# Kernel tuning notes

Measured on AMD Instinct MI355X. Metric: run time of the kernel, lower is better.

Reference implementation:

```python
import jax, jax.numpy as jnp
import numpy as np

T, B, E, H, DFF, K = 1024, 4, 512, 8, 2048, 31
D = E // H  # head_dim


def double_swish(x):
    # DoubleSwish: x * sigmoid(x - 1)
    return x * jax.nn.sigmoid(x - 1.0)


def ffn(x, w1, b1, w2, b2):
    # ScaledLinear -> ActivationBalancer(identity in eval) -> DoubleSwish -> ScaledLinear
    return double_swish(x @ w1.T + b1) @ w2.T + b2


def rel_shift(x):
    # x: (B, H, T, 2T-1) -> (B, H, T, T); out[b,h,i,j] = x[b,h,i, (T-1) - i + j]
    t = x.shape[2]
    idx = (t - 1) - jnp.arange(t)[:, None] + jnp.arange(t)[None, :]  # (T, T)
    return jnp.take_along_axis(x, idx[None, None], axis=-1)


def self_attn(x, pos_emb, wqkv, bqkv, wo, bo, wpos, u, v):
    # x: (T, B, E); Transformer-XL style rel-pos multi-head attention
    t, b, e = x.shape
    qkv = x @ wqkv.T + bqkv                       # (T, B, 3E)
    q, k, val = jnp.split(qkv, 3, axis=-1)
    q = q * (D ** -0.5)
    to_heads = lambda z: z.reshape(t, b, H, D).transpose(1, 2, 0, 3)  # (B,H,T,D)
    q, k, val = to_heads(q), to_heads(k), to_heads(val)
    # positional projection: (1, 2T-1, E) -> (1, H, D, 2T-1)
    p = (pos_emb @ wpos.T).reshape(1, 2 * t - 1, H, D).transpose(0, 2, 3, 1)
    ac = jnp.einsum('bhld,bhsd->bhls', q + u[None, :, None, :], k)
    bd = jnp.einsum('bhld,bhdm->bhlm', q + v[None, :, None, :], p)
    scores = ac + rel_shift(bd)                   # (B, H, T, T)
    attn = jax.nn.softmax(scores, axis=-1)
    out = jnp.einsum('bhls,bhsd->bhld', attn, val)
    out = out.transpose(2, 0, 1, 3).reshape(t, b, e)  # (T, B, E)
    return out @ wo.T + bo


def conv_module(x, pw1_w, pw1_b, dw_w, dw_b, pw2_w, pw2_b):
    # x: (T, B, C) -> (B, C, T)
    x = x.transpose(1, 2, 0)
    x = jnp.einsum('oc,bct->bot', pw1_w, x) + pw1_b[None, :, None]  # (B, 2C, T)
    a, g = jnp.split(x, 2, axis=1)
    x = a * jax.nn.sigmoid(g)                     # GLU over channel dim
    pad = (K - 1) // 2
    x = jax.lax.conv_general_dilated(
        x, dw_w, window_strides=(1,), padding=[(pad, pad)],
        dimension_numbers=('NCH', 'OIH', 'NCH'), feature_group_count=E)
    x = double_swish(x + dw_b[None, :, None])
    x = jnp.einsum('oc,bct->bot', pw2_w, x) + pw2_b[None, :, None]
    return x.transpose(2, 0, 1)                   # (T, B, C)


def basic_norm(x, log_eps):
    # BasicNorm: x * (mean(x^2, -1) + exp(eps))^{-0.5}
    return x * jax.lax.rsqrt(jnp.mean(x * x, axis=-1, keepdims=True) + jnp.exp(log_eps))


def setup_inputs() -> dict:
    key = jax.random.key(0)
    ks = jax.random.split(key, 24)
    std = jnp.float32(0.02)
    f = lambda k, s: jax.random.normal(k, s, jnp.float32)
    return dict(
        src=f(ks[0], (T, B, E)),
        pos_emb=f(ks[1], (1, 2 * T - 1, E)),
        in_proj_w=f(ks[2], (3 * E, E)) * std,
        in_proj_b=f(ks[3], (3 * E,)) * std,
        out_proj_w=f(ks[4], (E, E)) * std,
        out_proj_b=f(ks[5], (E,)) * std,
        linear_pos_w=f(ks[6], (E, E)) * std,
        pos_bias_u=f(ks[7], (H, D)) * jnp.float32(0.01),
        pos_bias_v=f(ks[8], (H, D)) * jnp.float32(0.01),
        ffm_w1=f(ks[9], (DFF, E)) * std, ffm_b1=f(ks[10], (DFF,)) * std,
        ffm_w2=f(ks[11], (E, DFF)) * std, ffm_b2=f(ks[12], (E,)) * std,
        ff_w1=f(ks[13], (DFF, E)) * std, ff_b1=f(ks[14], (DFF,)) * std,
        ff_w2=f(ks[15], (E, DFF)) * std, ff_b2=f(ks[16], (E,)) * std,
        conv_pw1_w=f(ks[17], (2 * E, E)) * std, conv_pw1_b=f(ks[18], (2 * E,)) * std,
        conv_dw_w=f(ks[19], (E, 1, K)) * std, conv_dw_b=f(ks[20], (E,)) * std,
        conv_pw2_w=f(ks[21], (E, E)) * std, conv_pw2_b=f(ks[22], (E,)) * std,
        norm_eps=jnp.array(np.log(0.25), jnp.float32),
    )


def reference(src, pos_emb, in_proj_w, in_proj_b, out_proj_w, out_proj_b,
              linear_pos_w, pos_bias_u, pos_bias_v,
              ffm_w1, ffm_b1, ffm_w2, ffm_b2,
              ff_w1, ff_b1, ff_w2, ff_b2,
              conv_pw1_w, conv_pw1_b, conv_dw_w, conv_dw_b, conv_pw2_w, conv_pw2_b,
              norm_eps):
    # macaron FFN
    x = src + ffn(src, ffm_w1, ffm_b1, ffm_w2, ffm_b2)
    # rel-pos self-attention
    x = x + self_attn(x, pos_emb, in_proj_w, in_proj_b, out_proj_w, out_proj_b,
                      linear_pos_w, pos_bias_u, pos_bias_v)
    # convolution module
    x = x + conv_module(x, conv_pw1_w, conv_pw1_b, conv_dw_w, conv_dw_b, conv_pw2_w, conv_pw2_b)
    # second FFN
    x = x + ffn(x, ff_w1, ff_b1, ff_w2, ff_b2)
    # balancer is identity in eval; final BasicNorm
    return basic_norm(x, norm_eps)
```

## Files before the change

kernel.cpp:

```cpp
#include <hip/hip_runtime.h>
#include <string.h>


#define T_ 1024
#define B_ 4
#define E_ 512
#define H_ 8
#define DFF_ 2048
#define KW_ 31

typedef unsigned short u16;
typedef unsigned int u32;
typedef __bf16 bf16x8 __attribute__((ext_vector_type(8)));
typedef float floatx4 __attribute__((ext_vector_type(4)));

__device__ __forceinline__ float b2f(u16 u) {
    return __uint_as_float(((u32)u) << 16);
}
__device__ __forceinline__ u16 f2b(float f) {
    u32 i = __float_as_uint(f);
    u32 r = (i + 0x7fffu + ((i >> 16) & 1u)) >> 16;
    return (u16)r;
}

__device__ __forceinline__ void glds16(const u16 *g, u16 *l) {
    __builtin_amdgcn_global_load_lds((const __attribute__((address_space(1))) void *)g,
                                     (__attribute__((address_space(3))) void *)l, 16, 0, 0);
}

__global__ __launch_bounds__(256) void fill_k(float *out, long long n, float val) {
    long long g = (long long)blockIdx.x * 256 + threadIdx.x;
    if (g < n) out[g] = val;
}

__global__ __launch_bounds__(256) void detect_k(const u16 *src16, int *flag) {
    __shared__ int sh[256];
    int tid = threadIdx.x;
    int cnt = 0;
    for (int i = tid; i < 4096; i += 256) {
        u16 x = src16[2 * i];
        int e = (x >> 7) & 0xFF;
        cnt += (e == 0 || (e >= 0x70 && e <= 0x8F)) ? 1 : 0;
    }
    sh[tid] = cnt;
    __syncthreads();
    for (int s = 128; s; s >>= 1) {
        if (tid < s) sh[tid] += sh[tid + s];
        __syncthreads();
    }
    if (tid == 0) *flag = (sh[0] < 2048) ? 1 : 0;
}

struct CVT {
    const void *in[24];
    long long pre[25];
};

__global__ __launch_bounds__(256) void convert_k(CVT c, u16 *dst, const int *flag,
                                                 long long total) {
    long long g8 = ((long long)blockIdx.x * 256 + threadIdx.x) * 8;
    if (g8 >= total) return;
    int s = 0;
#pragma unroll
    for (int i = 1; i < 25; i++) s += (g8 >= c.pre[i]) ? 1 : 0;
    long long l = g8 - c.pre[s];
    int f = *flag;
    if (g8 + 8 <= c.pre[s + 1]) {
        if (f) {
            const float *sp = (const float *)c.in[s] + l;
            float4 v0 = *(const float4 *)sp;
            float4 v1 = *(const float4 *)(sp + 4);
            uint4 o;
            o.x = (u32)f2b(v0.x) | ((u32)f2b(v0.y) << 16);
            o.y = (u32)f2b(v0.z) | ((u32)f2b(v0.w) << 16);
            o.z = (u32)f2b(v1.x) | ((u32)f2b(v1.y) << 16);
            o.w = (u32)f2b(v1.z) | ((u32)f2b(v1.w) << 16);
            *(uint4 *)(dst + g8) = o;
        } else {
            *(uint4 *)(dst + g8) = *(const uint4 *)((const u16 *)c.in[s] + l);
        }
    } else {
        for (int j = 0; j < 8; j++) {
            long long ge = g8 + j;
            if (ge >= total) break;
            int se = 0;
#pragma unroll
            for (int i = 1; i < 25; i++) se += (ge >= c.pre[i]) ? 1 : 0;
            long long le = ge - c.pre[se];
            dst[ge] = f ? f2b(((const float *)c.in[se])[le]) : ((const u16 *)c.in[se])[le];
        }
    }
}

struct GP {
    const u16 *A, *B;
    u16 *C;
    const u16 *bias;
    const void *resin;
    float *xr;
    u16 *xb;
    const u16 *ub, *vb;
    u16 *qu, *qv, *kh, *vt;
    int M, N, K, lda, ldb, ldc, mode, qcols, resin_f32;
    float qscale;
};

__device__ __forceinline__ void nt64_body(const GP &p, u16 *As, u16 *Bs,
                                          int bx, int by, int gx, int nb) {
    const int tid = threadIdx.x;
    const int wv = tid >> 6, ln = tid & 63;
    const int l16 = ln & 15, quad = ln >> 4;
    const int wm = (wv >> 2) << 5;
    const int wn = (wv & 3) << 4;
    const int lid = by * gx + bx;
    const int nid = (lid & 7) * (nb >> 3) + (lid >> 3);
    const int m0 = (nid / gx) << 6, n0 = (nid % gx) << 6;
    floatx4 zero = {0.f, 0.f, 0.f, 0.f};
    floatx4 acc[2];
    acc[0] = zero;
    acc[1] = zero;

    const int NT = p.K >> 6;

    const int srow = tid >> 3;
    const int sg = ((tid & 7) ^ (srow & 7)) << 3;
    int ra = m0 + srow;
    if (ra > p.M - 1) ra = p.M - 1;
    const u16 *Agp = p.A + (long long)ra * p.lda + sg;
    const u16 *Bgp = p.B + (long long)(n0 + srow) * p.ldb + sg;

    auto stage = [&](int bidx, int t) {
        const int k0 = t << 6;
        const int o = bidx << 12;
        glds16(Agp + k0, As + o + tid * 8);
        glds16(Bgp + k0, Bs + o + tid * 8);
    };
    auto ldregs = [&](int bidx, bf16x8 *af, bf16x8 *bv) {
        const int o = bidx << 12;
#pragma unroll
        for (int kk = 0; kk < 2; kk++) {
            const int swz = ((((kk << 2) | quad) ^ (l16 & 7)) << 3);
            bv[kk] = __builtin_bit_cast(bf16x8,
                *(const uint4 *)&Bs[o + ((wn + l16) << 6) + swz]);
#pragma unroll
            for (int mt = 0; mt < 2; mt++)
                af[kk * 2 + mt] = __builtin_bit_cast(bf16x8,
                    *(const uint4 *)&As[o + ((wm + (mt << 4) + l16) << 6) + swz]);
        }
    };
    auto mma = [&](const bf16x8 *af, const bf16x8 *bv) {
#pragma unroll
        for (int kk = 0; kk < 2; kk++)
#pragma unroll
            for (int mt = 0; mt < 2; mt++)
                acc[mt] = __builtin_amdgcn_mfma_f32_16x16x32_bf16(af[kk * 2 + mt], bv[kk],
                                                                  acc[mt], 0, 0, 0);
    };

    stage(0, 0);
    stage(1, 1);
    stage(2, 2);
    stage(3, 3);
    asm volatile("s_waitcnt vmcnt(4)" ::: "memory");
    __builtin_amdgcn_s_barrier();

    const int NP = NT >> 1;
    for (int ph = 0; ph < NP; ph++) {
        const int b0 = (ph << 1) & 3;
        bf16x8 af0[4], bv0[2], af1[4], bv1[2];
        ldregs(b0, af0, bv0);
        ldregs(b0 | 1, af1, bv1);
        __builtin_amdgcn_sched_barrier(0);
        asm volatile("s_waitcnt lgkmcnt(0)" ::: "memory");
        __builtin_amdgcn_s_barrier();
        __builtin_amdgcn_sched_barrier(0);
        const bool do_stage = (ph + 2 < NP);
        if (do_stage) {
            stage(b0, (ph << 1) + 4);
            stage(b0 | 1, (ph << 1) + 5);
        }
        mma(af0, bv0);
        mma(af1, bv1);
        if (ph + 1 < NP) {
            __builtin_amdgcn_sched_barrier(0);
            if (do_stage) {
                asm volatile("s_waitcnt vmcnt(4)" ::: "memory");
            } else {
                asm volatile("s_waitcnt vmcnt(0)" ::: "memory");
            }
            __builtin_amdgcn_s_barrier();
            __builtin_amdgcn_sched_barrier(0);
        }
    }

#pragma unroll
    for (int mt = 0; mt < 2; mt++) {
#pragma unroll
        for (int r = 0; r < 4; r++) {
            int gr = m0 + wm + (mt << 4) + (quad << 2) + r;
            int gc = n0 + wn + l16;
            bool oob = gr >= p.M;
            if (oob && p.mode != 3) continue;
            float y = 0.f;
            if (!oob) {
                y = acc[mt][r];
                if (p.bias) y += b2f(p.bias[gc]);
                if (gc < p.qcols) y *= p.qscale;
            }
            if (p.mode == 3) {
                p.C[((gc >> 6) << 17) + (gr << 6) + (gc & 63)] = f2b(y);
            } else if (p.mode == 0) {
                p.C[(long long)gr * p.ldc + gc] = f2b(y);
            } else if (p.mode == 1) {
                float s = 1.f / (1.f + __expf(1.f - y));
                p.C[(long long)gr * p.ldc + gc] = f2b(y * s);
            } else {
                long long idx = (long long)gr * p.ldc + gc;
                float rv = p.resin_f32 ? ((const float *)p.resin)[idx]
                                       : b2f(((const u16 *)p.resin)[idx]);
                float o = rv + y;
                p.xr[idx] = o;
                if (p.xb) p.xb[idx] = f2b(o);
            }
        }
    }
}

__device__ __forceinline__ void nt128_body(const GP &p, u16 *As, u16 *Bs,
                                           int bx, int by, int gx, int nb) {
    const int tid = threadIdx.x;
    const int wv = tid >> 6, ln = tid & 63;
    const int l16 = ln & 15, quad = ln >> 4;
    const int wm = (wv >> 2) << 6;
    const int wn = (wv & 3) << 5;
    const int lid = by * gx + bx;
    const int nid = (lid & 7) * (nb >> 3) + (lid >> 3);
    const int m0 = (nid / gx) << 7, n0 = (nid % gx) << 7;
    const int srow = tid >> 2;
    const int sg = ((tid & 3) ^ ((tid >> 3) & 3)) << 3;
    const u16 *Agp = p.A + (long long)(m0 + srow) * p.lda + sg;
    const u16 *Bgp = p.B + (long long)(n0 + srow) * p.ldb + sg;
    floatx4 zero = {0.f, 0.f, 0.f, 0.f};
    floatx4 acc[4][2];
#pragma unroll
    for (int i = 0; i < 4; i++)
#pragma unroll
        for (int j = 0; j < 2; j++) acc[i][j] = zero;

    const int rswz = ((quad ^ ((l16 >> 1) & 3)) << 3);
    const int NT = p.K >> 5;

    auto stage = [&](int bidx, int t) {
        const int k0 = t << 5;
        const int o = bidx << 12;
        glds16(Agp + k0, As + o + tid * 8);
        glds16(Bgp + k0, Bs + o + tid * 8);
    };
    auto ldregs = [&](int bidx, bf16x8 *av, bf16x8 *bv) {
        const int o = bidx << 12;
#pragma unroll
        for (int mt = 0; mt < 4; mt++)
            av[mt] = __builtin_bit_cast(bf16x8,
                *(const uint4 *)&As[o + ((wm + (mt << 4) + l16) << 5) + rswz]);
#pragma unroll
        for (int nt = 0; nt < 2; nt++)
            bv[nt] = __builtin_bit_cast(bf16x8,
                *(const uint4 *)&Bs[o + ((wn + (nt << 4) + l16) << 5) + rswz]);
    };
    auto mma = [&](const bf16x8 *av, const bf16x8 *bv) {
#pragma unroll
        for (int mt = 0; mt < 4; mt++)
#pragma unroll
            for (int nt = 0; nt < 2; nt++)
                acc[mt][nt] = __builtin_amdgcn_mfma_f32_16x16x32_bf16(av[mt], bv[nt],
                                                                      acc[mt][nt], 0, 0, 0);
    };

    stage(0, 0);
    stage(1, 1);
    stage(2, 2);
    stage(3, 3);
    asm volatile("s_waitcnt vmcnt(4)" ::: "memory");
    __builtin_amdgcn_s_barrier();

    const int NP = NT >> 1;
    for (int ph = 0; ph < NP; ph++) {
        const int b0 = (ph << 1) & 3;
        bf16x8 av0[4], bv0[2], av1[4], bv1[2];
        ldregs(b0, av0, bv0);
        ldregs(b0 | 1, av1, bv1);
        __builtin_amdgcn_sched_barrier(0);
        asm volatile("s_waitcnt lgkmcnt(0)" ::: "memory");
        __builtin_amdgcn_s_barrier();
        __builtin_amdgcn_sched_barrier(0);
        const bool do_stage = (ph + 2 < NP);
        if (do_stage) {
            stage(b0, (ph << 1) + 4);
            stage(b0 | 1, (ph << 1) + 5);
        }
        mma(av0, bv0);
        mma(av1, bv1);
        if (ph + 1 < NP) {
            __builtin_amdgcn_sched_barrier(0);
            if (do_stage) {
                asm volatile("s_waitcnt vmcnt(4)" ::: "memory");
            } else {
                asm volatile("s_waitcnt vmcnt(0)" ::: "memory");
            }
            __builtin_amdgcn_s_barrier();
            __builtin_amdgcn_sched_barrier(0);
        }
    }

#pragma unroll
    for (int mt = 0; mt < 4; mt++)
#pragma unroll
        for (int nt = 0; nt < 2; nt++)
#pragma unroll
            for (int r = 0; r < 4; r++) {
                int gr = m0 + wm + (mt << 4) + (quad << 2) + r;
                int gc = n0 + wn + (nt << 4) + l16;
                float y = acc[mt][nt][r];
                if (p.bias) y += b2f(p.bias[gc]);
                if (gc < p.qcols) y *= p.qscale;
                if (p.mode == 0) {
                    p.C[(long long)gr * p.ldc + gc] = f2b(y);
                } else if (p.mode == 1) {
                    float s = 1.f / (1.f + __expf(1.f - y));
                    p.C[(long long)gr * p.ldc + gc] = f2b(y * s);
                } else if (p.mode == 4) {
                    int t = gr >> 2, b = gr & 3;
                    if (gc < E_) {
                        int z = b * 8 + (gc >> 6);
                        long long oq = ((long long)z << 16) + (t << 6) + (gc & 63);
                        p.qu[oq] = f2b(y + b2f(p.ub[gc]));
                        p.qv[oq] = f2b(y + b2f(p.vb[gc]));
                    } else if (gc < 2 * E_) {
                        int c = gc - E_;
                        int z = b * 8 + (c >> 6);
                        p.kh[((long long)z << 16) + (t << 6) + (c & 63)] = f2b(y);
                    } else {
                        int c = gc - 2 * E_;
                        int z = b * 8 + (c >> 6);
                        p.vt[(long long)((z << 6) + (c & 63)) * T_ + t] = f2b(y);
                    }
                } else {
                    long long idx = (long long)gr * p.ldc + gc;
                    float rv = p.resin_f32 ? ((const float *)p.resin)[idx]
                                           : b2f(((const u16 *)p.resin)[idx]);
                    float o = rv + y;
                    p.xr[idx] = o;
                    if (p.xb) p.xb[idx] = f2b(o);
                }
            }
}

__global__ __launch_bounds__(512) void gemm_nt(GP p) {
    __shared__ __align__(16) u16 As[4 * 4096];
    __shared__ __align__(16) u16 Bs[4 * 4096];
    nt64_body(p, As, Bs, blockIdx.x, blockIdx.y, gridDim.x, gridDim.x * gridDim.y);
}

__global__ __launch_bounds__(512) void gemm_nt128(GP p) {
    __shared__ __align__(16) u16 As[4 * 4096];
    __shared__ __align__(16) u16 Bs[4 * 4096];
    nt128_body(p, As, Bs, blockIdx.x, blockIdx.y, gridDim.x, gridDim.x * gridDim.y);
}

__global__ __launch_bounds__(512) void gemm_w1pos(GP a, GP b) {
    __shared__ __align__(16) u16 As[4 * 4096];
    __shared__ __align__(16) u16 Bs[4 * 4096];
    if (blockIdx.z == 0) {
        nt128_body(a, As, Bs, blockIdx.x, blockIdx.y, 16, 512);
    } else {
        if (blockIdx.x >= 8) return;
        nt64_body(b, As, Bs, blockIdx.x, blockIdx.y, 8, 256);
    }
}

__global__ __launch_bounds__(512) void gemm_glu(const u16 *A, const u16 *W, const u16 *bias,
                                                u16 *ch) {
    __shared__ __align__(16) u16 As[3 * 4096];
    __shared__ __align__(16) u16 Ba[3 * 4096];
    __shared__ __align__(16) u16 Bg[3 * 4096];
    const int tid = threadIdx.x;
    const int wv = tid >> 6, ln = tid & 63;
    const int l16 = ln & 15, quad = ln >> 4;
    const int wm = (wv >> 2) << 5;
    const int wn = (wv & 3) << 4;
    const int gx = gridDim.x;
    const int nb = gx * gridDim.y;
    const int lid = blockIdx.y * gx + blockIdx.x;
    const int nid = (lid & 7) * (nb >> 3) + (lid >> 3);
    const int m0 = (nid / gx) << 6, n0 = (nid % gx) << 6;
    floatx4 zero = {0.f, 0.f, 0.f, 0.f};
    floatx4 aa[2], ag[2];
    aa[0] = zero; aa[1] = zero; ag[0] = zero; ag[1] = zero;

    const int NT = 8;
    const int srow = tid >> 3;
    const int sg = ((tid & 7) ^ (srow & 7)) << 3;
    const u16 *Agp = A + ((long long)(m0 + srow) << 9) + sg;
    const u16 *Bap = W + ((long long)(n0 + srow) << 9) + sg;
    const u16 *Bgp = W + ((long long)(E_ + n0 + srow) << 9) + sg;

    auto stage = [&](int bidx, int t) {
        const int k0 = t << 6;
        const int o = bidx << 12;
        glds16(Agp + k0, As + o + tid * 8);
        glds16(Bap + k0, Ba + o + tid * 8);
        glds16(Bgp + k0, Bg + o + tid * 8);
    };

    stage(0, 0);
    stage(1, 1);
    stage(2, 2);
    asm volatile("s_waitcnt vmcnt(6)" ::: "memory");
    __builtin_amdgcn_s_barrier();

    int cb = 0;
    for (int t = 0; t < NT; t++) {
        const int o = cb << 12;
#pragma unroll
        for (int kk = 0; kk < 2; kk++) {
            const int swz = ((((kk << 2) | quad) ^ (l16 & 7)) << 3);
            bf16x8 ba = __builtin_bit_cast(bf16x8,
                *(const uint4 *)&Ba[o + ((wn + l16) << 6) + swz]);
            bf16x8 bg = __builtin_bit_cast(bf16x8,
                *(const uint4 *)&Bg[o + ((wn + l16) << 6) + swz]);
#pragma unroll
            for (int mt = 0; mt < 2; mt++) {
                bf16x8 af = __builtin_bit_cast(bf16x8,
                    *(const uint4 *)&As[o + ((wm + (mt << 4) + l16) << 6) + swz]);
                aa[mt] = __builtin_amdgcn_mfma_f32_16x16x32_bf16(af, ba, aa[mt], 0, 0, 0);
                ag[mt] = __builtin_amdgcn_mfma_f32_16x16x32_bf16(af, bg, ag[mt], 0, 0, 0);
            }
        }
        if (t + 1 < NT) {
            __builtin_amdgcn_sched_barrier(0);
            __builtin_amdgcn_s_barrier();
            if (t + 3 < NT) {
                stage(cb, t + 3);
                asm volatile("s_waitcnt vmcnt(6)" ::: "memory");
            } else if (t + 2 < NT) {
                asm volatile("s_waitcnt vmcnt(3)" ::: "memory");
            } else {
                asm volatile("s_waitcnt vmcnt(0)" ::: "memory");
            }
            __builtin_amdgcn_s_barrier();
            __builtin_amdgcn_sched_barrier(0);
        }
        cb = (cb == 2) ? 0 : cb + 1;
    }

#pragma unroll
    for (int mt = 0; mt < 2; mt++) {
#pragma unroll
        for (int r = 0; r < 4; r++) {
            int gr = m0 + wm + (mt << 4) + (quad << 2) + r;
            int gc = n0 + wn + l16;
            float a = aa[mt][r] + b2f(bias[gc]);
            float g = ag[mt][r] + b2f(bias[E_ + gc]);
            ch[((long long)gr << 9) + gc] = f2b(a * (1.f / (1.f + __expf(-g))));
        }
    }
}

struct FK {
    const u16 *QU, *QV, *KH, *PPH, *VT;
    u16 *attno;
};

__global__ __launch_bounds__(256) void flash_k(FK p) {
    __shared__ __align__(16) u16 lds[2 * 16384 + 4608];

    const int tid = threadIdx.x;
    const int wv = tid >> 6, ln = tid & 63;
    const int l16 = ln & 15, quad = ln >> 4;
    const int lid = blockIdx.y * 16 + blockIdx.x;
    const int nid = (lid & 7) * 64 + (lid >> 3);
    const int zg = nid >> 4;
    const int i0 = (nid & 15) << 6;
    const u16 *kh0 = p.KH + (long long)zg * 65536;
    const u16 *ph0 = p.PPH + (long long)(zg & 7) * 131072;
    const u16 *vt0 = p.VT + (long long)zg * 65536;
    u16 *Pb = lds + 32768;

    auto stage = [&](int buf, int jt) {
        const int j0 = jt << 6;
        const int m_start = 960 - i0 + j0;
        u16 *Kh = lds + (buf << 14);
        u16 *Vt = Kh + 4096;
        u16 *Ph = Kh + 8192;
#pragma unroll
        for (int ps = 0; ps < 2; ps++) {
            int g = ps * 256 + tid;
            int row = g >> 3;
            int src = ((g & 7) ^ (row & 7)) << 3;
            glds16(kh0 + ((j0 + row) << 6) + src, Kh + g * 8);
            glds16(vt0 + (row << 10) + j0 + src, Vt + g * 8);
        }
#pragma unroll
        for (int ps = 0; ps < 4; ps++) {
            int g = ps * 256 + tid;
            int row = g >> 3;
            int src = ((g & 7) ^ (row & 7)) << 3;
            glds16(ph0 + ((m_start + row) << 6) + src, Ph + g * 8);
        }
    };

    const long long qoff = (long long)zg * 65536 + (long long)(i0 + (wv << 4) + l16) * 64 + (quad << 3);
    bf16x8 aqu[2], aqv[2];
#pragma unroll
    for (int kk = 0; kk < 2; kk++) {
        aqu[kk] = __builtin_bit_cast(bf16x8, *(const uint4 *)(p.QU + qoff + (kk << 5)));
        aqv[kk] = __builtin_bit_cast(bf16x8, *(const uint4 *)(p.QV + qoff + (kk << 5)));
    }

    stage(0, 0);
    asm volatile("s_waitcnt vmcnt(0)" ::: "memory");
    __builtin_amdgcn_s_barrier();

    float lacc[4];
    floatx4 accO[4];
    floatx4 zero = {0.f, 0.f, 0.f, 0.f};
#pragma unroll
    for (int e = 0; e < 4; e++) lacc[e] = 0.f;
#pragma unroll
    for (int i = 0; i < 4; i++) accO[i] = zero;

    const int r16q = quad << 2;

    for (int jt = 0; jt < 16; jt++) {
        if (jt + 1 < 16) stage((jt + 1) & 1, jt + 1);
        __builtin_amdgcn_sched_barrier(0);
        const int o = (jt & 1) << 14;
        const u16 *Kh = lds + o;
        const u16 *Vt = lds + o + 4096;
        const u16 *Ph = lds + o + 8192;

        floatx4 aS[4], aB[5];
#pragma unroll
        for (int i = 0; i < 4; i++) aS[i] = zero;
#pragma unroll
        for (int i = 0; i < 5; i++) aB[i] = zero;
        __builtin_amdgcn_s_setprio(1);
#pragma unroll
        for (int kk = 0; kk < 2; kk++) {
            const int swz = ((((kk << 2) | quad) ^ (l16 & 7)) << 3);
#pragma unroll
            for (int nt = 0; nt < 4; nt++) {
                bf16x8 bf = __builtin_bit_cast(bf16x8,
                    *(const uint4 *)&Kh[(((nt << 4) | l16) << 6) + swz]);
                aS[nt] = __builtin_amdgcn_mfma_f32_16x16x32_bf16(aqu[kk], bf, aS[nt], 0, 0, 0);
            }
#pragma unroll
            for (int rt = 0; rt < 5; rt++) {
                bf16x8 bf = __builtin_bit_cast(bf16x8,
                    *(const uint4 *)&Ph[((((rt + 3 - wv) << 4) | l16) << 6) + swz]);
                aB[rt] = __builtin_amdgcn_mfma_f32_16x16x32_bf16(aqv[kk], bf, aB[rt], 0, 0, 0);
            }
        }
        __builtin_amdgcn_s_setprio(0);

#pragma unroll
        for (int e = 0; e < 4; e++) {
            const int r16 = r16q + e;
            const int t = l16 + 15 - r16;
            const int srcl = (quad << 4) | (t & 15);
            const int carry = t >> 4;
            float ps = 0.f;
#pragma unroll
            for (int nt = 0; nt < 4; nt++) {
                float vlo = __shfl(aB[nt][e], srcl, 64);
                float vhi = __shfl(aB[nt + 1][e], srcl, 64);
                float bd = carry ? vhi : vlo;
                float pe = __expf(aS[nt][e] + bd);
                ps += pe;
                Pb[(((wv << 4) + r16) * 72) + (nt << 4) + l16] = f2b(pe);
            }
            lacc[e] += ps;
        }

        __builtin_amdgcn_s_setprio(1);
#pragma unroll
        for (int kk = 0; kk < 2; kk++) {
            const int swz = ((((kk << 2) | quad) ^ (l16 & 7)) << 3);
            bf16x8 ap = __builtin_bit_cast(bf16x8,
                *(const uint4 *)&Pb[(((wv << 4) | l16) * 72) + (kk << 5) + (quad << 3)]);
#pragma unroll
            for (int nd = 0; nd < 4; nd++) {
                bf16x8 bv = __builtin_bit_cast(bf16x8,
                    *(const uint4 *)&Vt[(((nd << 4) | l16) << 6) + swz]);
                accO[nd] = __builtin_amdgcn_mfma_f32_16x16x32_bf16(ap, bv, accO[nd], 0, 0, 0);
            }
        }
        __builtin_amdgcn_s_setprio(0);

        if (jt + 1 < 16) {
            __builtin_amdgcn_sched_barrier(0);
            __builtin_amdgcn_s_barrier();
            asm volatile("s_waitcnt vmcnt(0)" ::: "memory");
            __builtin_amdgcn_s_barrier();
            __builtin_amdgcn_sched_barrier(0);
        }
    }

    const int b = zg >> 3, h = zg & 7;
#pragma unroll
    for (int e = 0; e < 4; e++) {
#pragma unroll
        for (int msk = 1; msk < 16; msk <<= 1) lacc[e] += __shfl_xor(lacc[e], msk, 64);
        float inv = 1.f / lacc[e];
        int t = i0 + (wv << 4) + (quad << 2) + e;
#pragma unroll
        for (int nd = 0; nd < 4; nd++) {
            int d = (nd << 4) + l16;
            p.attno[(long long)(t * B_ + b) * E_ + h * 64 + d] = f2b(accO[nd][e] * inv);
        }
    }
}


__global__ __launch_bounds__(256) void dwconv_k(const u16 *ch, const u16 *w, const u16 *bias,
                                                u16 *cd) {
    const int cp = threadIdx.x;
    const int b = blockIdx.x >> 7;
    const int t0 = (blockIdx.x & 127) << 3;
    const int c0 = cp << 1;
    float in0[38], in1[38];
#pragma unroll
    for (int j = 0; j < 38; j++) {
        int tt = t0 - 15 + j;
        u32 v = 0;
        if (tt >= 0 && tt < T_) v = *(const u32 *)&ch[tt * 2048 + b * 512 + c0];
        in0[j] = b2f((u16)(v & 0xffff));
        in1[j] = b2f((u16)(v >> 16));
    }
    float w0[KW_], w1[KW_];
#pragma unroll
    for (int kk = 0; kk < KW_; kk++) {
        w0[kk] = b2f(w[c0 * KW_ + kk]);
        w1[kk] = b2f(w[c0 * KW_ + KW_ + kk]);
    }
    float bi0 = b2f(bias[c0]), bi1 = b2f(bias[c0 + 1]);
#pragma unroll
    for (int t = 0; t < 8; t++) {
        float a0 = bi0, a1 = bi1;
#pragma unroll
        for (int kk = 0; kk < KW_; kk++) {
            a0 += in0[t + kk] * w0[kk];
            a1 += in1[t + kk] * w1[kk];
        }
        float s0 = 1.f / (1.f + __expf(1.f - a0));
        float s1 = 1.f / (1.f + __expf(1.f - a1));
        u32 o = (u32)f2b(a0 * s0) | ((u32)f2b(a1 * s1) << 16);
        *(u32 *)&cd[(t0 + t) * 2048 + b * 512 + c0] = o;
    }
}

__global__ __launch_bounds__(256) void norm_k(const float *xr, const float *epsp, float *out) {
    int wv = threadIdx.x >> 6, ln = threadIdx.x & 63;
    long long row = blockIdx.x * 4 + wv;
    const float *x = xr + row * E_;
    float vals[8], ss = 0.f;
#pragma unroll
    for (int i = 0; i < 8; i++) {
        vals[i] = x[ln + (i << 6)];
        ss += vals[i] * vals[i];
    }
#pragma unroll
    for (int m = 32; m; m >>= 1) ss += __shfl_xor(ss, m, 64);
    float sc = rsqrtf(ss * (1.f / (float)E_) + __expf(epsp[0]));
    float *o = out + row * E_;
#pragma unroll
    for (int i = 0; i < 8; i++) o[ln + (i << 6)] = vals[i] * sc;
}


extern "C" void kernel_launch(void *const *d_in, const int *in_sizes, int n_in,
                              void *d_out, int out_size, void *d_ws, size_t ws_size,
                              hipStream_t stream) {
    const size_t MB = (size_t)1 << 20;
    static const long long EXPECT[24] = {
        2097152, 1048064, 786432, 1536, 262144, 512, 262144, 512, 512,
        1048576, 2048, 1048576, 512, 1048576, 2048, 1048576, 512,
        524288, 1024, 15872, 512, 262144, 512, 1};
    const size_t NEED = 93 * MB;

    float code = 0.f;
    if (n_in != 24) {
        code = 1000.f + (float)n_in;
    } else {
        for (int i = 0; i < 24; i++) {
            if ((long long)in_sizes[i] != EXPECT[i]) { code = 2000.f + 64.f * i; break; }
        }
    }
    if (code == 0.f && out_size != 2097152) code = 3000.f;
    if (code == 0.f && ws_size < NEED) code = 5000.f + (float)(ws_size / MB);
    if (code != 0.f) {
        long long n = (long long)out_size;
        fill_k<<<dim3((unsigned)((n + 255) / 256)), dim3(256), 0, stream>>>((float *)d_out, n, code);
        return;
    }

    char *w = (char *)d_ws;
    int *flag = (int *)(w + 0);
    u16 *cv = (u16 *)(w + 1 * MB);
    float *xr = (float *)(w + 21 * MB);
    u16 *xb = (u16 *)(w + 29 * MB);
    u16 *h1 = (u16 *)(w + 33 * MB);
    u16 *pph = (u16 *)(w + 63 * MB);
    u16 *QU = (u16 *)(w + 65 * MB);
    u16 *QV = (u16 *)(w + 69 * MB);
    u16 *KH = (u16 *)(w + 73 * MB);
    u16 *VT = (u16 *)(w + 77 * MB);
    u16 *attno = (u16 *)(w + 81 * MB);
    u16 *ch = (u16 *)(w + 85 * MB);
    u16 *cd = (u16 *)(w + 89 * MB);

    detect_k<<<dim3(1), dim3(256), 0, stream>>>((const u16 *)d_in[0], flag);
    CVT c;
    c.pre[0] = 0;
    for (int i = 0; i < 24; i++) {
        c.in[i] = d_in[i];
        c.pre[i + 1] = c.pre[i] + in_sizes[i];
    }
    long long total = c.pre[24];
    long long groups = (total + 7) / 8;
    convert_k<<<dim3((unsigned)((groups + 255) / 256)), dim3(256), 0, stream>>>(c, cv, flag, total);

    const u16 *src = cv + c.pre[0];
    const u16 *pos_emb = cv + c.pre[1];
    const u16 *w_qkv = cv + c.pre[2];
    const u16 *b_qkv = cv + c.pre[3];
    const u16 *w_o = cv + c.pre[4];
    const u16 *b_o = cv + c.pre[5];
    const u16 *w_pos = cv + c.pre[6];
    const u16 *u_bias = cv + c.pre[7];
    const u16 *v_bias = cv + c.pre[8];
    const u16 *ffm_w1 = cv + c.pre[9];
    const u16 *ffm_b1 = cv + c.pre[10];
    const u16 *ffm_w2 = cv + c.pre[11];
    const u16 *ffm_b2 = cv + c.pre[12];
    const u16 *ff_w1 = cv + c.pre[13];
    const u16 *ff_b1 = cv + c.pre[14];
    const u16 *ff_w2 = cv + c.pre[15];
    const u16 *ff_b2 = cv + c.pre[16];
    const u16 *pw1_w = cv + c.pre[17];
    const u16 *pw1_b = cv + c.pre[18];
    const u16 *dw_w = cv + c.pre[19];
    const u16 *dw_b = cv + c.pre[20];
    const u16 *pw2_w = cv + c.pre[21];
    const u16 *pw2_b = cv + c.pre[22];

    auto mk = [](const void *A, int lda, const void *B, int ldb, void *C, int ldc,
                 const void *bias, int M, int N, int K, int mode) {
        GP p;
        memset(&p, 0, sizeof(p));
        p.A = (const u16 *)A; p.B = (const u16 *)B; p.C = (u16 *)C; p.bias = (const u16 *)bias;
        p.M = M; p.N = N; p.K = K; p.lda = lda; p.ldb = ldb; p.ldc = ldc; p.mode = mode;
        p.qscale = 1.f;
        return p;
    };
    auto launch = [&](GP p) {
        dim3 g((p.N + 63) / 64, (p.M + 63) / 64, 1);
        gemm_nt<<<g, dim3(512), 0, stream>>>(p);
    };
    auto launch128 = [&](GP p) {
        dim3 g(p.N >> 7, p.M >> 7, 1);
        gemm_nt128<<<g, dim3(512), 0, stream>>>(p);
    };

    const int M = T_ * B_;

    {
        GP a = mk(src, E_, ffm_w1, E_, h1, DFF_, ffm_b1, M, DFF_, E_, 1);
        GP b = mk(pos_emb, E_, w_pos, E_, pph, E_, nullptr, 2 * T_ - 1, E_, E_, 3);
        gemm_w1pos<<<dim3(16, 32, 2), dim3(512), 0, stream>>>(a, b);
    }
    { GP p = mk(h1, DFF_, ffm_w2, DFF_, nullptr, E_, ffm_b2, M, E_, DFF_, 2);
      p.resin = d_in[0]; p.resin_f32 = 1; p.xr = xr; p.xb = xb; launch(p); }

    { GP p = mk(xb, E_, w_qkv, E_, nullptr, 3 * E_, b_qkv, M, 3 * E_, E_, 4);
      p.qcols = E_; p.qscale = 0.125f;
      p.ub = u_bias; p.vb = v_bias; p.qu = QU; p.qv = QV; p.kh = KH; p.vt = VT;
      launch128(p); }

    {
        FK f;
        f.QU = QU; f.QV = QV; f.KH = KH; f.PPH = pph; f.VT = VT; f.attno = attno;
        flash_k<<<dim3(16, 32), dim3(256), 0, stream>>>(f);
    }

    { GP p = mk(attno, E_, w_o, E_, nullptr, E_, b_o, M, E_, E_, 2);
      p.resin = xr; p.resin_f32 = 1; p.xr = xr; p.xb = xb; launch(p); }

    gemm_glu<<<dim3(8, 64), dim3(512), 0, stream>>>(xb, pw1_w, pw1_b, ch);
    dwconv_k<<<dim3(512), dim3(256), 0, stream>>>(ch, dw_w, dw_b, cd);
    { GP p = mk(cd, E_, pw2_w, E_, nullptr, E_, pw2_b, M, E_, E_, 2);
      p.resin = xr; p.resin_f32 = 1; p.xr = xr; p.xb = xb; launch(p); }

    { GP p = mk(xb, E_, ff_w1, E_, h1, DFF_, ff_b1, M, DFF_, E_, 1); launch128(p); }
    { GP p = mk(h1, DFF_, ff_w2, DFF_, nullptr, E_, ff_b2, M, E_, DFF_, 2);
      p.resin = xr; p.resin_f32 = 1; p.xr = xr; p.xb = nullptr; launch(p); }

    norm_k<<<dim3(M / 4), dim3(256), 0, stream>>>(xr, (const float *)d_in[23], (float *)d_out);
}
```

Baseline: 331.1 us.

## Split-K the FFN down-projection GEMMs with a separate combine kernel

Both FFN second GEMMs (K=2048, N=512) are replaced by a split-K kernel that computes two K halves in parallel into fp32 partial buffers. A new elementwise combine kernel then adds the partials, bias and residual and writes the fp32 and bf16 activations. This doubles the number of blocks for a narrow-N GEMM to improve occupancy across CUs. The cost is an extra kernel launch plus fp32 partial traffic, and part1 reuses workspace that overlaps the QU buffer.

After: 343.0 us. 1.04x slower.

```diff
diff --git a/kernel.cpp b/kernel.cpp
--- a/kernel.cpp
+++ b/kernel.cpp
@@ -378,6 +378,105 @@
     }
 }
 
+__global__ __launch_bounds__(512) void gemm_splitk(const u16 *A, const u16 *Bw,
+                                                   float *p0, float *p1) {
+    __shared__ __align__(16) u16 As[3 * 4096];
+    __shared__ __align__(16) u16 Bs[3 * 4096];
+    const int tid = threadIdx.x;
+    const int wv = tid >> 6, ln = tid & 63;
+    const int l16 = ln & 15, quad = ln >> 4;
+    const int wm = (wv >> 2) << 5;
+    const int wn = (wv & 3) << 4;
+    const int lid = blockIdx.y * 8 + blockIdx.x;
+    const int nid = (lid & 7) * 64 + (lid >> 3);
+    const int m0 = (nid >> 3) << 6, n0 = (nid & 7) << 6;
+    const int koff = blockIdx.z << 10;
+    float *part = blockIdx.z ? p1 : p0;
+    floatx4 zero = {0.f, 0.f, 0.f, 0.f};
+    floatx4 acc[2];
+    acc[0] = zero;
+    acc[1] = zero;
+
+    const int NT = 16;
+    const int srow = tid >> 3;
+    const int sg = ((tid & 7) ^ (srow & 7)) << 3;
+    const u16 *Agp = A + (long long)(m0 + srow) * 2048 + koff + sg;
+    const u16 *Bgp = Bw + (long long)(n0 + srow) * 2048 + koff + sg;
+
+    auto stage = [&](int bidx, int t) {
+        const int k0 = t << 6;
+        const int o = bidx << 12;
+        glds16(Agp + k0, As + o + tid * 8);
+        glds16(Bgp + k0, Bs + o + tid * 8);
+    };
+
+    stage(0, 0);
+    stage(1, 1);
+    stage(2, 2);
+    asm volatile("s_waitcnt vmcnt(4)" ::: "memory");
+    __builtin_amdgcn_s_barrier();
+
+    int cb = 0;
+    for (int t = 0; t < NT; t++) {
+        const int o = cb << 12;
+#pragma unroll
+        for (int kk = 0; kk < 2; kk++) {
+            const int swz = ((((kk << 2) | quad) ^ (l16 & 7)) << 3);
+            bf16x8 bfv = __builtin_bit_cast(bf16x8,
+                *(const uint4 *)&Bs[o + ((wn + l16) << 6) + swz]);
+#pragma unroll
+            for (int mt = 0; mt < 2; mt++) {
+                bf16x8 af = __builtin_bit_cast(bf16x8,
+                    *(const uint4 *)&As[o + ((wm + (mt << 4) + l16) << 6) + swz]);
+                acc[mt] = __builtin_amdgcn_mfma_f32_16x16x32_bf16(af, bfv, acc[mt], 0, 0, 0);
+            }
+        }
+        if (t + 1 < NT) {
+            __builtin_amdgcn_sched_barrier(0);
+            __builtin_amdgcn_s_barrier();
+            if (t + 3 < NT) {
+                stage(cb, t + 3);
+                asm volatile("s_waitcnt vmcnt(4)" ::: "memory");
+            } else if (t + 2 < NT) {
+                asm volatile("s_waitcnt vmcnt(2)" ::: "memory");
+            } else {
+                asm volatile("s_waitcnt vmcnt(0)" ::: "memory");
+            }
+            __builtin_amdgcn_s_barrier();
+            __builtin_amdgcn_sched_barrier(0);
+        }
+        cb = (cb == 2) ? 0 : cb + 1;
+    }
+
+#pragma unroll
+    for (int mt = 0; mt < 2; mt++)
+#pragma unroll
+        for (int r = 0; r < 4; r++) {
+            int gr = m0 + wm + (mt << 4) + (quad << 2) + r;
+            int gc = n0 + wn + l16;
+            part[((long long)gr << 9) + gc] = acc[mt][r];
+        }
+}
+
+__global__ __launch_bounds__(256) void combine2_k(const float *p0, const float *p1,
+                                                  const u16 *bias, const void *resin,
+                                                  int resin_f32, float *xr, u16 *xb) {
+    int gid = (blockIdx.x * 256 + threadIdx.x) * 4;
+    float4 a = *(const float4 *)(p0 + gid);
+    float4 b = *(const float4 *)(p1 + gid);
+    int gc = gid & 511;
+#pragma unroll
+    for (int i = 0; i < 4; i++) {
+        float y = (i == 0 ? a.x + b.x : i == 1 ? a.y + b.y : i == 2 ? a.z + b.z : a.w + b.w);
+        y += b2f(bias[gc + i]);
+        float rv = resin_f32 ? ((const float *)resin)[gid + i]
+                             : b2f(((const u16 *)resin)[gid + i]);
+        float o = rv + y;
+        xr[gid + i] = o;
+        if (xb) xb[gid + i] = f2b(o);
+    }
+}
+
 __global__ __launch_bounds__(512) void gemm_glu(const u16 *A, const u16 *W, const u16 *bias,
                                                 u16 *ch) {
     __shared__ __align__(16) u16 As[3 * 4096];
@@ -710,8 +809,10 @@
     float *xr = (float *)(w + 21 * MB);
     u16 *xb = (u16 *)(w + 29 * MB);
     u16 *h1 = (u16 *)(w + 33 * MB);
+    float *part0 = (float *)(w + 49 * MB);
     u16 *pph = (u16 *)(w + 63 * MB);
     u16 *QU = (u16 *)(w + 65 * MB);
+    float *part1 = (float *)(w + 65 * MB);
     u16 *QV = (u16 *)(w + 69 * MB);
     u16 *KH = (u16 *)(w + 73 * MB);
     u16 *VT = (u16 *)(w + 77 * MB);
@@ -779,8 +880,9 @@
         GP b = mk(pos_emb, E_, w_pos, E_, pph, E_, nullptr, 2 * T_ - 1, E_, E_, 3);
         gemm_w1pos<<<dim3(16, 32, 2), dim3(512), 0, stream>>>(a, b);
     }
-    { GP p = mk(h1, DFF_, ffm_w2, DFF_, nullptr, E_, ffm_b2, M, E_, DFF_, 2);
-      p.resin = d_in[0]; p.resin_f32 = 1; p.xr = xr; p.xb = xb; launch(p); }
+    gemm_splitk<<<dim3(8, 64, 2), dim3(512), 0, stream>>>(h1, ffm_w2, part0, part1);
+    combine2_k<<<dim3(2048), dim3(256), 0, stream>>>(part0, part1, ffm_b2,
+                                                     d_in[0], 1, xr, xb);
 
     { GP p = mk(xb, E_, w_qkv, E_, nullptr, 3 * E_, b_qkv, M, 3 * E_, E_, 4);
       p.qcols = E_; p.qscale = 0.125f;
@@ -802,8 +904,9 @@
       p.resin = xr; p.resin_f32 = 1; p.xr = xr; p.xb = xb; launch(p); }
 
     { GP p = mk(xb, E_, ff_w1, E_, h1, DFF_, ff_b1, M, DFF_, E_, 1); launch128(p); }
-    { GP p = mk(h1, DFF_, ff_w2, DFF_, nullptr, E_, ff_b2, M, E_, DFF_, 2);
-      p.resin = xr; p.resin_f32 = 1; p.xr = xr; p.xb = nullptr; launch(p); }
+    gemm_splitk<<<dim3(8, 64, 2), dim3(512), 0, stream>>>(h1, ff_w2, part0, part1);
+    combine2_k<<<dim3(2048), dim3(256), 0, stream>>>(part0, part1, ff_b2,
+                                                     xr, 1, xr, nullptr);
 
     norm_k<<<dim3(M / 4), dim3(256), 0, stream>>>(xr, (const float *)d_in[23], (float *)d_out);
 }
```
